# Optimization experiments

Measured on AMD Instinct MI355X. Metric: run time of the kernel, lower is better.

## Reference

```python
import jax, jax.numpy as jnp
import numpy as np

VOCAB, HID, EMB = 32000, 512, 256
N, L = 256, 512


def setup_inputs() -> dict:
    key = jax.random.key(0)
    ks = jax.random.split(key, 6)
    X = jax.random.randint(ks[0], (N, L), 0, VOCAB)
    emb = jax.random.normal(ks[1], (VOCAB, EMB), dtype=jnp.float32) * 0.02
    # torch Linear: y = x @ W.T + b, W shape (out, in)
    Whh_w = jax.random.normal(ks[2], (HID, HID), dtype=jnp.float32) * (1.0 / np.sqrt(HID))
    Whh_b = jnp.zeros((HID,), dtype=jnp.float32)
    Wxh_w = jax.random.normal(ks[3], (HID, EMB), dtype=jnp.float32) * (1.0 / np.sqrt(EMB))
    Wxh_b = jnp.zeros((HID,), dtype=jnp.float32)
    return {"X": X, "emb": emb, "Whh_w": Whh_w, "Whh_b": Whh_b,
            "Wxh_w": Wxh_w, "Wxh_b": Wxh_b}


def reference(X, emb, Whh_w, Whh_b, Wxh_w, Wxh_b):
    # X: (N, L) int ids -> last hidden state (N, H)
    E = emb[X]                       # (N, L, E) embedding lookup
    # precompute input projection for all timesteps (one big GEMM)
    XP = jnp.einsum('nle,he->nlh', E, Wxh_w) + Wxh_b  # (N, L, H)
    h0 = jnp.zeros((X.shape[0], Whh_w.shape[0]), dtype=emb.dtype)

    def step(h, xp_t):
        # xp_t: (N, H) at time t
        h_new = jnp.tanh(h @ Whh_w.T + Whh_b + xp_t)
        return h_new, None

    h_last, _ = jax.lax.scan(step, h0, jnp.swapaxes(XP, 0, 1))  # scan over L
    return h_last
```

## Files before the change

kernel.cpp:

```cpp
#include <hip/hip_runtime.h>
#include <hip/hip_bf16.h>
#include <math.h>

#define N_B    256
#define L_SEQ  512
#define HID    512
#define EMB_D  256

#define NGROUPS 16
#define GWGS    8

#define ESW_SHORTS_PER_BLK 8192
#define ESW_BYTES  ((size_t)NGROUPS * L_SEQ * ESW_SHORTS_PER_BLK * 2)
#define EX_UINTS_PER_SLOT (16 * HID)
#define EX_BYTES   ((size_t)2 * NGROUPS * EX_UINTS_PER_SLOT * 4)

typedef short v8s __attribute__((ext_vector_type(8)));
typedef float v4f __attribute__((ext_vector_type(4)));

static __device__ __forceinline__ unsigned short bf_bits(__hip_bfloat16 h) {
    union { __hip_bfloat16 b; unsigned short u; } c; c.b = h; return c.u;
}
static __device__ __forceinline__ void split_hilo(float v, short& hi, short& lo) {
    const __hip_bfloat16 h = __float2bfloat16(v);
    hi = (short)bf_bits(h);
    lo = (short)bf_bits(__float2bfloat16(v - __bfloat162float(h)));
}
static __device__ __forceinline__ void cvt8_hilo(const float* __restrict__ p,
                                                 v8s& hi, v8s& lo) {
    #pragma unroll
    for (int i = 0; i < 8; ++i) { short h, l; split_hilo(p[i], h, l); hi[i] = h; lo[i] = l; }
}
static __device__ __forceinline__ void gl_lds16(const short* g, short* l) {
    __builtin_amdgcn_global_load_lds(
        (const __attribute__((address_space(1))) unsigned int*)g,
        (__attribute__((address_space(3))) unsigned int*)l, 16, 0, 0);
}
static __device__ __forceinline__ float tanh_fast(float x) {
    const float z = __expf(2.0f * x);
    return 1.0f - 2.0f / (z + 1.0f);
}

__global__ __launch_bounds__(256) void esw_build(
    const int* __restrict__ X, const float* __restrict__ emb,
    short* __restrict__ Esw)
{
    const int bid = blockIdx.x;
    const int g = bid >> 9, t = bid & 511;
    short* base = Esw + (size_t)bid * ESW_SHORTS_PER_BLK;
    #pragma unroll
    for (int h = 0; h < 2; ++h) {
        const int f    = threadIdx.x + h * 256;
        const int kk   = f >> 6, lane = f & 63;
        const int m    = lane & 15, qp = lane >> 4;
        const int idx  = X[(g * 16 + m) * L_SEQ + t];
        const float* src = emb + (size_t)idx * EMB_D + kk * 32 + qp * 8;
        v8s hi8, lo8;
        cvt8_hilo(src, hi8, lo8);
        short* d = base + (size_t)(kk * 64 + lane) * 8;
        *(v8s*)d          = hi8;
        *(v8s*)(d + 4096) = lo8;
    }
}

__global__ __launch_bounds__(256, 1) void rnn_scan5(
    const float* __restrict__ Whh,
    const float* __restrict__ Whh_b,
    const float* __restrict__ Wxh,
    const float* __restrict__ Wxh_b,
    const short* __restrict__ Esw,
    unsigned int* __restrict__ ex,
    float* __restrict__ out)
{
    const int bid  = blockIdx.x;
    const int g    = bid & 15;
    const int j    = bid >> 4;
    const int tid  = threadIdx.x;
    const int w    = tid >> 6;
    const int l    = tid & 63;
    const int lo16 = l & 15;
    const int q    = l >> 4;
    const int cbase = j * 64 + w * 16;
    const int nbase = g * 16;

    __shared__ short ldsbuf[49152];
    __shared__ unsigned int tp[4][256];
    short* lds_h = ldsbuf;
    short* lds_e = ldsbuf + 32768;

    v8s bhi[16], blo[16];
    {
        const float* wp = Whh + (long)(cbase + lo16) * HID + q * 8;
        #pragma unroll
        for (int kk = 0; kk < 16; ++kk) cvt8_hilo(wp + kk * 32, bhi[kk], blo[kk]);
    }
    v8s xhi[8], xlo[8];
    {
        const float* wp = Wxh + (long)(cbase + lo16) * EMB_D + q * 8;
        #pragma unroll
        for (int kk = 0; kk < 8; ++kk) cvt8_hilo(wp + kk * 32, xhi[kk], xlo[kk]);
    }
    const int hcol = cbase + lo16;
    const float bias = Whh_b[hcol] + Wxh_b[hcol];

    const int region = (2 * j + (w >> 1)) * 512 + (w & 1) * 256;

    unsigned int* ex0 = ex + (size_t)g * EX_UINTS_PER_SLOT;
    unsigned int* ex1 = ex + (size_t)(NGROUPS + g) * EX_UINTS_PER_SLOT;
    const short* esrc = Esw + (size_t)(g * 512) * ESW_SHORTS_PER_BLK;

    #pragma unroll
    for (int c = 0; c < 4; ++c)
        gl_lds16(esrc + (w * 4 + c) * 512 + l * 8, lds_e + (w * 4 + c) * 512);
    __syncthreads();

    for (int t = 0; t < L_SEQ; ++t) {
        const int P = t & 1;
        short* lh = lds_h + P * 16384;
        short* le = lds_e + P * 8192;
        unsigned int* exsrc = P ? ex1 : ex0;
        unsigned int* exdst = P ? ex0 : ex1;

        if (t + 1 < L_SEQ) {
            const short* eb = esrc + (size_t)(t + 1) * ESW_SHORTS_PER_BLK;
            short* leN = lds_e + (P ^ 1) * 8192;
            #pragma unroll
            for (int c = 0; c < 4; ++c)
                gl_lds16(eb + (w * 4 + c) * 512 + l * 8, leN + (w * 4 + c) * 512);
        }

        v4f acc0 = {0,0,0,0}, acc1 = {0,0,0,0}, acc2 = {0,0,0,0};
        #pragma unroll
        for (int kk = 0; kk < 8; ++kk) {
            v8s ah = *(const v8s*)(le + (kk * 64 + l) * 8);
            v8s al = *(const v8s*)(le + 4096 + (kk * 64 + l) * 8);
            acc0 = __builtin_amdgcn_mfma_f32_16x16x32_bf16(ah, xhi[kk], acc0, 0, 0, 0);
            acc1 = __builtin_amdgcn_mfma_f32_16x16x32_bf16(ah, xlo[kk], acc1, 0, 0, 0);
            acc2 = __builtin_amdgcn_mfma_f32_16x16x32_bf16(al, xhi[kk], acc2, 0, 0, 0);
        }

        unsigned long long hv64[16];
        {
            const unsigned long long* hs = (const unsigned long long*)exsrc;
            const unsigned long long tagmask = 0x0001000000010000ull;
            const unsigned long long want = ((t >> 1) & 1) ? tagmask : 0ull;
            for (;;) {
                #pragma unroll
                for (int s = 0; s < 16; ++s)
                    hv64[s] = __hip_atomic_load(hs + s * 256 + tid,
                                                __ATOMIC_RELAXED,
                                                __HIP_MEMORY_SCOPE_AGENT);
                unsigned long long bad = 0;
                #pragma unroll
                for (int s = 0; s < 16; ++s) bad |= (hv64[s] ^ want) & tagmask;
                if (__all(bad == 0)) break;
            }
        }

        {
            unsigned int* lh_hi = (unsigned int*)lh;
            unsigned int* lh_lo = lh_hi + 4096;
            #pragma unroll
            for (int s = 0; s < 16; ++s) {
                const int o = s * 256 + tid;
                const unsigned int w0 = (unsigned int)hv64[s];
                const unsigned int w1 = (unsigned int)(hv64[s] >> 32);
                lh_hi[o] = (w0 & 0xffffu) | (w1 << 16);
                lh_lo[o] = (w0 >> 16)     | (w1 & 0xffff0000u);
            }
        }
        __syncthreads();

        #pragma unroll
        for (int kk = 0; kk < 16; ++kk) {
            v8s ah = *(const v8s*)(lh + (kk * 64 + l) * 8);
            v8s al = *(const v8s*)(lh + 8192 + (kk * 64 + l) * 8);
            acc0 = __builtin_amdgcn_mfma_f32_16x16x32_bf16(ah, bhi[kk], acc0, 0, 0, 0);
            acc1 = __builtin_amdgcn_mfma_f32_16x16x32_bf16(ah, blo[kk], acc1, 0, 0, 0);
            acc2 = __builtin_amdgcn_mfma_f32_16x16x32_bf16(al, bhi[kk], acc2, 0, 0, 0);
        }

        if (t < L_SEQ - 1) {
            const unsigned int wtag = (unsigned int)(((t + 1) >> 1) & 1) << 16;
            unsigned int* myt = tp[w];
            #pragma unroll
            for (int r = 0; r < 4; ++r) {
                const int m = q * 4 + r;
                const float pre = acc0[r] + acc1[r] + acc2[r] + bias;
                const float hv = tanh_fast(pre);
                short hi, lo; split_hilo(hv, hi, lo);
                unsigned int word = (unsigned int)(unsigned short)hi
                                  | ((unsigned int)(unsigned short)lo << 16);
                word = (word & 0xFFFEFFFFu) | wtag;
                myt[(m + 16 * (lo16 >> 3)) * 8 + (lo16 & 7)] = word;
            }
            asm volatile("s_waitcnt lgkmcnt(0)" ::: "memory");
            #pragma unroll
            for (int k = 0; k < 4; ++k) {
                const unsigned int val = myt[k * 64 + l];
                __hip_atomic_store(exdst + region + k * 64 + l, val,
                                   __ATOMIC_RELAXED, __HIP_MEMORY_SCOPE_AGENT);
            }
        } else {
            #pragma unroll
            for (int r = 0; r < 4; ++r) {
                const int m = q * 4 + r;
                const float pre = acc0[r] + acc1[r] + acc2[r] + bias;
                out[(long)(nbase + m) * HID + hcol] = tanh_fast(pre);
            }
        }
    }
}

extern "C" void kernel_launch(void* const* d_in, const int* in_sizes, int n_in,
                              void* d_out, int out_size, void* d_ws, size_t ws_size,
                              hipStream_t stream) {
    const int*   X     = (const int*)d_in[0];
    const float* emb   = (const float*)d_in[1];
    const float* Whh   = (const float*)d_in[2];
    const float* Whh_b = (const float*)d_in[3];
    const float* Wxh   = (const float*)d_in[4];
    const float* Wxh_b = (const float*)d_in[5];

    char* ws = (char*)d_ws;
    short*        Esw = (short*)ws;
    unsigned int* ex  = (unsigned int*)(ws + ESW_BYTES);

    hipMemsetAsync(ex, 0x00, EX_BYTES / 2, stream);
    hipMemsetAsync((char*)ex + EX_BYTES / 2, 0xFF, EX_BYTES / 2, stream);

    esw_build<<<dim3(NGROUPS * L_SEQ), dim3(256), 0, stream>>>(X, emb, Esw);
    rnn_scan5<<<dim3(NGROUPS * GWGS), dim3(256), 0, stream>>>(
        Whh, Whh_b, Wxh, Wxh_b, Esw, ex, (float*)d_out);
}
```

Baseline: 1.507 ms.

## Detect same-XCC groups at runtime and use L2-scoped sync loads/stores

Adds a runtime handshake where each workgroup records its XCC id and probes whether plain stores are visible to sc0 loads among the 8 blocks of its group. If every block in the group sits on the same XCC and the probe passes, the scan uses cheaper non-system-coherent loads and stores for the per-step hidden-state exchange; otherwise it falls back to the original agent-scope atomics. This aims to cut the per-timestep cross-workgroup communication latency. The cost is an extra memset and a startup handshake, and correctness now rests on a hardware-placement assumption that is only checked empirically.

```diff
diff --git a/kernel.cpp b/kernel.cpp
--- a/kernel.cpp
+++ b/kernel.cpp
@@ -14,6 +14,7 @@
 #define ESW_BYTES  ((size_t)NGROUPS * L_SEQ * ESW_SHORTS_PER_BLK * 2)
 #define EX_UINTS_PER_SLOT (16 * HID)
 #define EX_BYTES   ((size_t)2 * NGROUPS * EX_UINTS_PER_SLOT * 4)
+#define CTL_BYTES  4096
 
 typedef short v8s __attribute__((ext_vector_type(8)));
 typedef float v4f __attribute__((ext_vector_type(4)));
@@ -39,6 +40,22 @@
 static __device__ __forceinline__ float tanh_fast(float x) {
     const float z = __expf(2.0f * x);
     return 1.0f - 2.0f / (z + 1.0f);
+}
+
+static __device__ __forceinline__ void st_sc1(unsigned int* p, unsigned int v) {
+    __hip_atomic_store(p, v, __ATOMIC_RELAXED, __HIP_MEMORY_SCOPE_AGENT);
+}
+static __device__ __forceinline__ unsigned int ld_sc1(const unsigned int* p) {
+    return __hip_atomic_load(p, __ATOMIC_RELAXED, __HIP_MEMORY_SCOPE_AGENT);
+}
+static __device__ __forceinline__ unsigned int ld_sc0(const unsigned int* p) {
+    unsigned int v;
+    asm volatile("global_load_dword %0, %1, off sc0\n\ts_waitcnt vmcnt(0)"
+                 : "=v"(v) : "v"(p) : "memory");
+    return v;
+}
+static __device__ __forceinline__ void st_plain(unsigned int* p, unsigned int v) {
+    asm volatile("global_store_dword %0, %1, off" :: "v"(p), "v"(v) : "memory");
 }
 
 __global__ __launch_bounds__(256) void esw_build(
@@ -63,19 +80,14 @@
     }
 }
 
-__global__ __launch_bounds__(256, 1) void rnn_scan5(
-    const float* __restrict__ Whh,
-    const float* __restrict__ Whh_b,
-    const float* __restrict__ Wxh,
-    const float* __restrict__ Wxh_b,
-    const short* __restrict__ Esw,
-    unsigned int* __restrict__ ex,
-    float* __restrict__ out)
+template<bool FAST>
+static __device__ __forceinline__ void scan_loop(
+    const float* __restrict__ Whh, const float* __restrict__ Whh_b,
+    const float* __restrict__ Wxh, const float* __restrict__ Wxh_b,
+    const short* __restrict__ Esw, unsigned int* __restrict__ ex,
+    float* __restrict__ out, short* __restrict__ ldsbuf,
+    unsigned int (*__restrict__ tp)[256], const int g, const int j, const int tid)
 {
-    const int bid  = blockIdx.x;
-    const int g    = bid & 15;
-    const int j    = bid >> 4;
-    const int tid  = threadIdx.x;
     const int w    = tid >> 6;
     const int l    = tid & 63;
     const int lo16 = l & 15;
@@ -83,8 +95,6 @@
     const int cbase = j * 64 + w * 16;
     const int nbase = g * 16;
 
-    __shared__ short ldsbuf[49152];
-    __shared__ unsigned int tp[4][256];
     short* lds_h = ldsbuf;
     short* lds_e = ldsbuf + 32768;
 
@@ -144,16 +154,31 @@
             const unsigned long long* hs = (const unsigned long long*)exsrc;
             const unsigned long long tagmask = 0x0001000000010000ull;
             const unsigned long long want = ((t >> 1) & 1) ? tagmask : 0ull;
-            for (;;) {
-                #pragma unroll
-                for (int s = 0; s < 16; ++s)
-                    hv64[s] = __hip_atomic_load(hs + s * 256 + tid,
-                                                __ATOMIC_RELAXED,
-                                                __HIP_MEMORY_SCOPE_AGENT);
-                unsigned long long bad = 0;
-                #pragma unroll
-                for (int s = 0; s < 16; ++s) bad |= (hv64[s] ^ want) & tagmask;
-                if (__all(bad == 0)) break;
+            if (FAST) {
+                for (;;) {
+                    #pragma unroll
+                    for (int s = 0; s < 16; ++s)
+                        asm volatile("global_load_dwordx2 %0, %1, off sc0"
+                                     : "=v"(hv64[s]) : "v"(hs + s * 256 + tid));
+                    asm volatile("s_waitcnt vmcnt(0)" ::: "memory");
+                    __builtin_amdgcn_sched_barrier(0);
+                    unsigned long long bad = 0;
+                    #pragma unroll
+                    for (int s = 0; s < 16; ++s) bad |= (hv64[s] ^ want) & tagmask;
+                    if (__all(bad == 0)) break;
+                }
+            } else {
+                for (;;) {
+                    #pragma unroll
+                    for (int s = 0; s < 16; ++s)
+                        hv64[s] = __hip_atomic_load(hs + s * 256 + tid,
+                                                    __ATOMIC_RELAXED,
+                                                    __HIP_MEMORY_SCOPE_AGENT);
+                    unsigned long long bad = 0;
+                    #pragma unroll
+                    for (int s = 0; s < 16; ++s) bad |= (hv64[s] ^ want) & tagmask;
+                    if (__all(bad == 0)) break;
+                }
             }
         }
 
@@ -197,9 +222,10 @@
             asm volatile("s_waitcnt lgkmcnt(0)" ::: "memory");
             #pragma unroll
             for (int k = 0; k < 4; ++k) {
-                const unsigned int val = myt[k * 64 + l];
-                __hip_atomic_store(exdst + region + k * 64 + l, val,
-                                   __ATOMIC_RELAXED, __HIP_MEMORY_SCOPE_AGENT);
+                const unsigned int val = tp[w][k * 64 + l];
+                unsigned int* p = exdst + region + k * 64 + l;
+                if (FAST) st_plain(p, val);
+                else      st_sc1(p, val);
             }
         } else {
             #pragma unroll
@@ -210,6 +236,90 @@
             }
         }
     }
+}
+
+__global__ __launch_bounds__(256, 1) void rnn_scan7(
+    const float* __restrict__ Whh,
+    const float* __restrict__ Whh_b,
+    const float* __restrict__ Wxh,
+    const float* __restrict__ Wxh_b,
+    const short* __restrict__ Esw,
+    unsigned int* __restrict__ ex,
+    unsigned int* __restrict__ ctl,
+    float* __restrict__ out)
+{
+    const int bid = blockIdx.x;
+    const int g   = bid & 15;
+    const int j   = bid >> 4;
+    const int tid = threadIdx.x;
+
+    __shared__ short ldsbuf[49152];
+    __shared__ unsigned int tp[4][256];
+    __shared__ int s_fast;
+
+    if (tid == 0) {
+        int allok = 0;
+        if (ctl != nullptr) {
+            unsigned int* det  = ctl;
+            unsigned int* tokA = ctl + 128;
+            unsigned int* tokB = ctl + 256;
+            unsigned int* prm  = ctl + 384;
+            unsigned int* vot  = ctl + 512;
+            unsigned int xcc;
+            asm volatile("s_getreg_b32 %0, hwreg(HW_REG_XCC_ID)" : "=s"(xcc));
+            st_sc1(det + bid, 0x100u | (xcc & 0xffu));
+            unsigned int ids[8];
+            for (int jj = 0; jj < 8; ++jj) {
+                unsigned int v;
+                do { v = ld_sc1(det + jj * 16 + g); } while (v == 0xFFFFFFFFu);
+                ids[jj] = v;
+            }
+            bool same = true;
+            for (int jj = 1; jj < 8; ++jj) same &= (ids[jj] == ids[0]);
+            int ok = 0;
+            if (same) {
+                for (int jj = 0; jj < 8; ++jj) {
+                    (void)ld_sc0(tokA + jj * 16 + g);
+                    (void)ld_sc0(tokB + jj * 16 + g);
+                }
+                st_sc1(prm + bid, 1u);
+                for (int jj = 0; jj < 8; ++jj)
+                    while (ld_sc1(prm + jj * 16 + g) == 0xFFFFFFFFu) {}
+                int budget = 1 << 13;
+                st_plain(tokA + bid, 0xA5A5A5A5u);
+                ok = 1;
+                for (int jj = 0; jj < 8 && ok; ++jj) {
+                    unsigned int v;
+                    do { v = ld_sc0(tokA + jj * 16 + g); }
+                    while (v != 0xA5A5A5A5u && --budget > 0);
+                    if (v != 0xA5A5A5A5u) ok = 0;
+                }
+                if (ok) {
+                    st_plain(tokB + bid, 0x5A5A5A5Au);
+                    for (int jj = 0; jj < 8 && ok; ++jj) {
+                        unsigned int v;
+                        do { v = ld_sc0(tokB + jj * 16 + g); }
+                        while (v != 0x5A5A5A5Au && --budget > 0);
+                        if (v != 0x5A5A5A5Au) ok = 0;
+                    }
+                }
+            }
+            st_sc1(vot + bid, ok ? 2u : 1u);
+            allok = 1;
+            for (int jj = 0; jj < 8; ++jj) {
+                unsigned int v;
+                do { v = ld_sc1(vot + jj * 16 + g); } while (v == 0xFFFFFFFFu);
+                allok &= (v == 2u) ? 1 : 0;
+            }
+        }
+        s_fast = allok;
+    }
+    __syncthreads();
+
+    if (s_fast)
+        scan_loop<true >(Whh, Whh_b, Wxh, Wxh_b, Esw, ex, out, ldsbuf, tp, g, j, tid);
+    else
+        scan_loop<false>(Whh, Whh_b, Wxh, Wxh_b, Esw, ex, out, ldsbuf, tp, g, j, tid);
 }
 
 extern "C" void kernel_launch(void* const* d_in, const int* in_sizes, int n_in,
@@ -225,11 +335,15 @@
     char* ws = (char*)d_ws;
     short*        Esw = (short*)ws;
     unsigned int* ex  = (unsigned int*)(ws + ESW_BYTES);
+    unsigned int* ctl = nullptr;
+    if (ws_size >= ESW_BYTES + EX_BYTES + CTL_BYTES)
+        ctl = (unsigned int*)(ws + ESW_BYTES + EX_BYTES);
 
     hipMemsetAsync(ex, 0x00, EX_BYTES / 2, stream);
     hipMemsetAsync((char*)ex + EX_BYTES / 2, 0xFF, EX_BYTES / 2, stream);
+    if (ctl) hipMemsetAsync(ctl, 0xFF, CTL_BYTES, stream);
 
     esw_build<<<dim3(NGROUPS * L_SEQ), dim3(256), 0, stream>>>(X, emb, Esw);
-    rnn_scan5<<<dim3(NGROUPS * GWGS), dim3(256), 0, stream>>>(
-        Whh, Whh_b, Wxh, Wxh_b, Esw, ex, (float*)d_out);
-}
+    rnn_scan7<<<dim3(NGROUPS * GWGS), dim3(256), 0, stream>>>(
+        Whh, Whh_b, Wxh, Wxh_b, Esw, ex, ctl, (float*)d_out);
+}
```

After: 2.471 ms. 64.0% more time.
